# Optimization experiments

Measured on AMD Instinct MI355X. Metric: run time of the kernel, lower is better.

## Reference

```python
import jax, jax.numpy as jnp
import numpy as np

D_MODEL = 1024
N_HEADS = 16
HEAD_DIM = D_MODEL // N_HEADS


def setup_inputs() -> dict:
    key = jax.random.key(0)
    ks = jax.random.split(key, 5)
    B, S = 4, 2048
    scale = 1.0 / np.sqrt(D_MODEL)
    return {
        "x": jax.random.normal(ks[0], (B, S, D_MODEL), dtype=jnp.float32),
        "W_q": jax.random.normal(ks[1], (D_MODEL, D_MODEL), dtype=jnp.float32) * scale,
        "W_k": jax.random.normal(ks[2], (D_MODEL, D_MODEL), dtype=jnp.float32) * scale,
        "W_v": jax.random.normal(ks[3], (D_MODEL, D_MODEL), dtype=jnp.float32) * scale,
        "W_o": jax.random.normal(ks[4], (D_MODEL, D_MODEL), dtype=jnp.float32) * scale,
    }


def reference(x, W_q, W_k, W_v, W_o):
    B, S, _ = x.shape
    # nn.Linear(d,d,bias=False): y = x @ W.T ; W stored as (out,in)
    def proj(W):
        y = jnp.einsum('bsd,ed->bse', x, W)
        return y.reshape(B, S, N_HEADS, HEAD_DIM).transpose(0, 2, 1, 3)  # (B,H,S,Dh)
    q, k, v = proj(W_q), proj(W_k), proj(W_v)
    scores = jnp.einsum('bhqd,bhkd->bhqk', q, k) / np.sqrt(HEAD_DIM)
    causal = jnp.tril(jnp.ones((S, S), dtype=bool))  # (S,S)
    scores = jnp.where(causal[None, None], scores, -jnp.inf)
    attn = jax.nn.softmax(scores, axis=-1)
    heads = jnp.einsum('bhqk,bhkd->bhqd', attn, v)
    concat = heads.transpose(0, 2, 1, 3).reshape(B, S, D_MODEL)
    return jnp.einsum('bsd,ed->bse', concat, W_o)
```

## Files before the change

### kernel.cpp

```cpp
#include <hip/hip_runtime.h>
#include <hip/hip_bf16.h>

#define D_MODEL 1024
#define N_HEADS 16
#define HEAD_DIM 64
#define BATCH 4
#define SEQ 2048
#define M_ROWS (BATCH * SEQ)

typedef __attribute__((ext_vector_type(8))) __bf16 bf16x8;
typedef __attribute__((ext_vector_type(8))) short short8;
typedef __attribute__((ext_vector_type(4))) float f32x4;

static __device__ __forceinline__ unsigned short f2bf_rne(float f) {
  unsigned int u = __float_as_uint(f);
  u += 0x7FFFu + ((u >> 16) & 1u);
  return (unsigned short)(u >> 16);
}

#if __has_builtin(__builtin_amdgcn_exp2f)
#define EXP2F(x) __builtin_amdgcn_exp2f(x)
#else
#define EXP2F(x) exp2f(x)
#endif

static __device__ __forceinline__ void gl_lds16(const unsigned short* g, unsigned short* l) {
  __builtin_amdgcn_global_load_lds((const __attribute__((address_space(1))) unsigned int*)g,
                                   (__attribute__((address_space(3))) unsigned int*)l, 16, 0, 0);
}

#define BAR() asm volatile("s_barrier" ::: "memory")
#define WAIT_LGKM0() asm volatile("s_waitcnt lgkmcnt(0)" ::: "memory")
#define WAIT_VM(N) asm volatile("s_waitcnt vmcnt(" #N ")" ::: "memory")

__global__ __launch_bounds__(256) void cvt_all(const float* __restrict__ x,
                                               const float* __restrict__ wq,
                                               const float* __restrict__ wk,
                                               const float* __restrict__ wv,
                                               const float* __restrict__ wo,
                                               unsigned short* __restrict__ xb,
                                               unsigned short* __restrict__ wqb,
                                               unsigned short* __restrict__ wkb,
                                               unsigned short* __restrict__ wvb,
                                               unsigned short* __restrict__ wob) {
  const int bid = blockIdx.x;
  const float* src;
  unsigned short* dst;
  int i;
  if (bid < 8192) {
    src = x; dst = xb; i = bid * 256 + threadIdx.x;
  } else {
    int r = bid - 8192;
    int w = r >> 10;
    i = (r & 1023) * 256 + threadIdx.x;
    switch (w) {
      case 0: src = wq; dst = wqb; break;
      case 1: src = wk; dst = wkb; break;
      case 2: src = wv; dst = wvb; break;
      default: src = wo; dst = wob; break;
    }
  }
  float4 f = reinterpret_cast<const float4*>(src)[i];
  ushort4 o;
  o.x = f2bf_rne(f.x); o.y = f2bf_rne(f.y); o.z = f2bf_rne(f.z); o.w = f2bf_rne(f.w);
  reinterpret_cast<ushort4*>(dst)[i] = o;
}

__global__ __launch_bounds__(512, 2) void qkv_gemm8(const unsigned short* __restrict__ A,
                                                    const unsigned short* __restrict__ Wq,
                                                    const unsigned short* __restrict__ Wk,
                                                    const unsigned short* __restrict__ Wv,
                                                    unsigned short* __restrict__ Qo,
                                                    unsigned short* __restrict__ Ko,
                                                    unsigned short* __restrict__ Vt) {
  __shared__ __align__(16) unsigned short smem[65536];

  const int bid = blockIdx.x;
  const int wgid = (bid & 7) * 48 + (bid >> 3);
  const int widx = wgid >> 7;
  const int rem = wgid & 127;
  const int bm = rem >> 2, bn = rem & 3;

  const unsigned short* Bw = (widx == 0) ? Wq : (widx == 1) ? Wk : Wv;

  const int t = threadIdx.x;
  const int wave = t >> 6, lane = t & 63;
  const int wmi = wave >> 2, wni = wave & 3;
  const int lr = lane & 15, quad = lane >> 4;

  const int r0 = t >> 3, c0 = (t & 7) ^ (r0 & 7);
  const int s1 = t + 512;
  const int r1 = s1 >> 3, c1 = (s1 & 7) ^ (r1 & 7);
  const unsigned short* Asrc0 = A + (size_t)(bm * 256 + r0) * D_MODEL + c0 * 8;
  const unsigned short* Asrc1 = A + (size_t)(bm * 256 + r1) * D_MODEL + c1 * 8;
  const unsigned short* Bsrc0 = Bw + (size_t)(bn * 256 + r0) * D_MODEL + c0 * 8;
  const unsigned short* Bsrc1 = Bw + (size_t)(bn * 256 + r1) * D_MODEL + c1 * 8;

  auto stageA = [&](int kt, int buf, int half) {
    unsigned short* dst = &smem[(buf * 2 + half) * 8192];
    const size_t go = (size_t)half * (128 * D_MODEL) + kt * 64;
    gl_lds16(Asrc0 + go, dst + t * 8);
    gl_lds16(Asrc1 + go, dst + s1 * 8);
  };
  auto stageB = [&](int kt, int buf, int half) {
    unsigned short* dst = &smem[32768 + (buf * 2 + half) * 8192];
    const size_t go = (size_t)half * (128 * D_MODEL) + kt * 64;
    gl_lds16(Bsrc0 + go, dst + t * 8);
    gl_lds16(Bsrc1 + go, dst + s1 * 8);
  };

  f32x4 acc[8][4] = {};
  bf16x8 bfrag[4][2];

  stageA(0, 0, 0); stageA(0, 0, 1);
  stageB(0, 0, 0); stageB(0, 0, 1);
  stageB(1, 1, 0); stageB(1, 1, 1);
  WAIT_VM(4);
  BAR();

  const int brow0 = (wni & 1) * 64;
  for (int j = 0; j < 8; ++j) {
#pragma unroll
    for (int tb = 0; tb < 2; ++tb) {
      const unsigned short* As = &smem[(tb * 2 + wmi) * 8192];
      const unsigned short* Bs = &smem[32768 + (tb * 2 + (wni >> 1)) * 8192];
#pragma unroll
      for (int qd = 0; qd < 4; ++qd) {
        const int p = tb * 4 + qd;
        if (qd == 0) {
#pragma unroll
          for (int n = 0; n < 4; ++n)
#pragma unroll
            for (int ks = 0; ks < 2; ++ks) {
              const int row = brow0 + n * 16 + lr;
              bfrag[n][ks] = __builtin_bit_cast(
                  bf16x8, *reinterpret_cast<const short8*>(
                              &Bs[row * 64 + (((ks * 4 + quad) ^ (row & 7)) * 8)]));
            }
        }
        bf16x8 af[2][2];
#pragma unroll
        for (int mi = 0; mi < 2; ++mi)
#pragma unroll
          for (int ks = 0; ks < 2; ++ks) {
            const int row = (qd * 2 + mi) * 16 + lr;
            af[mi][ks] = __builtin_bit_cast(
                bf16x8, *reinterpret_cast<const short8*>(
                            &As[row * 64 + (((ks * 4 + quad) ^ (row & 7)) * 8)]));
          }
        if (p == 0) stageA(2 * j + 1, 1, 0);
        if (p == 1) { stageA(2 * j + 1, 1, 1); if (j < 7) stageB(2 * j + 2, 0, 0); }
        if (p == 2) { if (j < 7) stageB(2 * j + 2, 0, 1); }
        if (p == 4) { if (j < 7) stageA(2 * j + 2, 0, 0); }
        if (p == 5) { if (j < 7) { stageA(2 * j + 2, 0, 1); stageB(2 * j + 3, 1, 0); } }
        if (p == 6) { if (j < 7) stageB(2 * j + 3, 1, 1); }
        BAR();
        WAIT_LGKM0();
        __builtin_amdgcn_s_setprio(1);
#pragma unroll
        for (int mi = 0; mi < 2; ++mi)
#pragma unroll
          for (int n = 0; n < 4; ++n)
#pragma unroll
            for (int ks = 0; ks < 2; ++ks)
              acc[qd * 2 + mi][n] = __builtin_amdgcn_mfma_f32_16x16x32_bf16(
                  af[mi][ks], bfrag[n][ks], acc[qd * 2 + mi][n], 0, 0, 0);
        __builtin_amdgcn_s_setprio(0);
        if (p == 3) { if (j < 7) { WAIT_VM(4); } else { WAIT_VM(0); } }
        if (p == 7) { if (j < 7) { WAIT_VM(4); } }
        BAR();
      }
    }
  }

  if (widx < 2) {
    unsigned short* Cp = (widx == 0) ? Qo : Ko;
    const float sc = (widx == 0) ? 0.18033688f : 1.0f;
#pragma unroll
    for (int m = 0; m < 8; ++m) {
#pragma unroll
      for (int n = 0; n < 4; ++n) {
        const int col = bn * 256 + wni * 64 + n * 16 + lr;
#pragma unroll
        for (int r = 0; r < 4; ++r) {
          const int row = bm * 256 + wmi * 128 + m * 16 + quad * 4 + r;
          Cp[(size_t)row * D_MODEL + col] = f2bf_rne(acc[m][n][r] * sc);
        }
      }
    }
  } else {
    const int b = bm >> 3;
    const int s0 = (bm & 7) * 256;
#pragma unroll
    for (int h = 0; h < 2; ++h) {
      __syncthreads();
      if (wmi == h) {
#pragma unroll
        for (int n = 0; n < 4; ++n) {
          const int d = wni * 64 + n * 16 + lr;
#pragma unroll
          for (int m = 0; m < 8; ++m) {
#pragma unroll
            for (int r = 0; r < 4; ++r) {
              const int srow = m * 16 + quad * 4 + r;
              smem[d * 136 + srow] = f2bf_rne(acc[m][n][r]);
            }
          }
        }
      }
      __syncthreads();
#pragma unroll
      for (int i = 0; i < 8; ++i) {
        const int c = i * 512 + t;
        const int d = c >> 4, s8 = (c & 15) * 8;
        uint4 v = *reinterpret_cast<const uint4*>(&smem[d * 136 + s8]);
        const int h2 = bn * 4 + (d >> 6);
        const size_t rowbase = (size_t)(b * N_HEADS + h2) * HEAD_DIM + (d & 63);
        *reinterpret_cast<uint4*>(Vt + rowbase * SEQ + s0 + h * 128 + s8) = v;
      }
    }
  }
}

__global__ __launch_bounds__(256) void gemm_bt_f32(const unsigned short* __restrict__ A,
                                                   const unsigned short* __restrict__ Bw,
                                                   float* __restrict__ Cp,
                                                   int M, int N, int K) {
  __shared__ __align__(16) unsigned short smem[16384];
  const int t = threadIdx.x;
  const int bn = blockIdx.x, bm = blockIdx.y;
  const int wave = t >> 6, lane = t & 63;
  const int wm = (wave >> 1) * 64, wn = (wave & 1) * 64;
  const int lr = lane & 15, quad = lane >> 4;
  const int rxor = (lr >> 1) & 3;

  const int g0 = wave * 128 + lane, g1 = g0 + 64;
  const int r0 = g0 >> 2, c0 = (((g0 & 3) ^ ((r0 >> 1) & 3)) << 3);
  const int r1 = g1 >> 2, c1 = (((g1 & 3) ^ ((r1 >> 1) & 3)) << 3);
  const unsigned short* Arow0 = A + (size_t)(bm * 128 + r0) * K + c0;
  const unsigned short* Arow1 = A + (size_t)(bm * 128 + r1) * K + c1;
  const unsigned short* Brow0 = Bw + (size_t)(bn * 128 + r0) * K + c0;
  const unsigned short* Brow1 = Bw + (size_t)(bn * 128 + r1) * K + c1;

  f32x4 acc[4][4] = {};

  gl_lds16(Arow0, &smem[g0 * 8]);
  gl_lds16(Arow1, &smem[g1 * 8]);
  gl_lds16(Brow0, &smem[4096 + g0 * 8]);
  gl_lds16(Brow1, &smem[4096 + g1 * 8]);
  __syncthreads();

  for (int it = 0; it < 32; it++) {
    const int cur = (it & 1) * 8192;
    if (it + 1 < 32) {
      const int nxt = 8192 - cur;
      const int k1 = (it + 1) * 32;
      gl_lds16(Arow0 + k1, &smem[nxt + g0 * 8]);
      gl_lds16(Arow1 + k1, &smem[nxt + g1 * 8]);
      gl_lds16(Brow0 + k1, &smem[nxt + 4096 + g0 * 8]);
      gl_lds16(Brow1 + k1, &smem[nxt + 4096 + g1 * 8]);
    }
    const unsigned short* As = &smem[cur];
    const unsigned short* Bs = &smem[cur + 4096];

    bf16x8 af[4], bfr[4];
#pragma unroll
    for (int mt = 0; mt < 4; mt++)
      af[mt] = __builtin_bit_cast(
          bf16x8,
          *reinterpret_cast<const short8*>(&As[(wm + mt * 16 + lr) * 32 + (quad ^ rxor) * 8]));
#pragma unroll
    for (int nt = 0; nt < 4; nt++)
      bfr[nt] = __builtin_bit_cast(
          bf16x8,
          *reinterpret_cast<const short8*>(&Bs[(wn + nt * 16 + lr) * 32 + (quad ^ rxor) * 8]));
#pragma unroll
    for (int mt = 0; mt < 4; mt++)
#pragma unroll
      for (int nt = 0; nt < 4; nt++)
        acc[mt][nt] = __builtin_amdgcn_mfma_f32_16x16x32_bf16(af[mt], bfr[nt], acc[mt][nt], 0, 0, 0);
    __syncthreads();
  }

#pragma unroll
  for (int mt = 0; mt < 4; mt++) {
#pragma unroll
    for (int nt = 0; nt < 4; nt++) {
      int col = bn * 128 + wn + nt * 16 + lr;
#pragma unroll
      for (int r = 0; r < 4; r++) {
        int row = bm * 128 + wm + mt * 16 + quad * 4 + r;
        Cp[(size_t)row * N + col] = acc[mt][nt][r];
      }
    }
  }
}

__global__ __launch_bounds__(512, 4) void attn_causal(const unsigned short* __restrict__ Q,
                                                      const unsigned short* __restrict__ Km,
                                                      const unsigned short* __restrict__ Vt,
                                                      unsigned short* __restrict__ O) {
  __shared__ __align__(16) unsigned short Kv[2][2][64 * 64];
  __shared__ __align__(16) unsigned short Ps[8][16 * 72];

  const int bid = blockIdx.x;
  const int p = bid & 7;
  const int h = (bid >> 3) & 15;
  const int b = bid >> 7;

  const int t = threadIdx.x;
  const int wave = t >> 6, lane = t & 63;
  const int lr = lane & 15, quad = lane >> 4;
  const int cxor = lr & 7;

  const size_t base = (size_t)b * SEQ * D_MODEL + h * HEAD_DIM;
  const unsigned short* Qb = Q + base;
  const unsigned short* Kb = Km + base;
  const unsigned short* Vb = Vt + (size_t)(b * N_HEADS + h) * HEAD_DIM * SEQ;
  unsigned short* pw = &Ps[wave][0];

  const int srow = t >> 3;
  const int scol = ((t & 7) ^ (srow & 7)) << 3;
  const unsigned short* Kg = Kb + (size_t)srow * D_MODEL + scol;
  const unsigned short* Vg = Vb + (size_t)srow * SEQ + scol;

  for (int ph = 0; ph < 2; ph++) {
    const int qt = ph ? (15 - p) : p;
    const int m0 = qt * 128 + wave * 16;
    const int ntiles = (qt + 1) * 2;

    bf16x8 qf[2];
#pragma unroll
    for (int kk = 0; kk < 2; kk++)
      qf[kk] = __builtin_bit_cast(
          bf16x8,
          *reinterpret_cast<const short8*>(Qb + (size_t)(m0 + lr) * D_MODEL + kk * 32 + quad * 8));

    f32x4 o_acc[4] = {};
    float lsum[4] = {};

    gl_lds16(Kg, &Kv[0][0][t * 8]);
    gl_lds16(Vg, &Kv[0][1][t * 8]);

    for (int kt = 0; kt < ntiles; kt++) {
      const int cur = kt & 1;
      const int kv0 = kt * 64;
      __syncthreads();
      if (kt + 1 < ntiles) {
        gl_lds16(Kg + (size_t)(kv0 + 64) * D_MODEL, &Kv[1 - cur][0][t * 8]);
        gl_lds16(Vg + kv0 + 64, &Kv[1 - cur][1][t * 8]);
      }
      const unsigned short* Ks = &Kv[cur][0][0];
      const unsigned short* Vs = &Kv[cur][1][0];

      f32x4 sAcc[4] = {};
      __builtin_amdgcn_s_setprio(1);
#pragma unroll
      for (int kk = 0; kk < 2; kk++) {
        bf16x8 kf[4];
#pragma unroll
        for (int j = 0; j < 4; j++)
          kf[j] = __builtin_bit_cast(
              bf16x8, *reinterpret_cast<const short8*>(
                          &Ks[(j * 16 + lr) * 64 + ((kk * 4 + quad) ^ cxor) * 8]));
#pragma unroll
        for (int j = 0; j < 4; j++)
          sAcc[j] = __builtin_amdgcn_mfma_f32_16x16x32_bf16(qf[kk], kf[j], sAcc[j], 0, 0, 0);
      }
      __builtin_amdgcn_s_setprio(0);

      asm volatile("s_waitcnt lgkmcnt(0)" ::: "memory");
      const bool needmask = (kv0 + 63 > m0);
#pragma unroll
      for (int r = 0; r < 4; r++) {
        const int qpos = m0 + quad * 4 + r;
        float e[4];
#pragma unroll
        for (int j = 0; j < 4; j++) e[j] = EXP2F(sAcc[j][r]);
        if (needmask) {
#pragma unroll
          for (int j = 0; j < 4; j++)
            if (kv0 + j * 16 + lr > qpos) e[j] = 0.f;
        }
        lsum[r] += (e[0] + e[1]) + (e[2] + e[3]);
        unsigned short* pr = &pw[(quad * 4 + r) * 72];
#pragma unroll
        for (int j = 0; j < 4; j++) pr[j * 16 + lr] = f2bf_rne(e[j]);
      }
      asm volatile("s_waitcnt lgkmcnt(0)" ::: "memory");

      __builtin_amdgcn_s_setprio(1);
#pragma unroll
      for (int kk = 0; kk < 2; kk++) {
        bf16x8 pf = __builtin_bit_cast(
            bf16x8, *reinterpret_cast<const short8*>(&pw[lr * 72 + kk * 32 + quad * 8]));
#pragma unroll
        for (int c = 0; c < 4; c++) {
          bf16x8 vv = __builtin_bit_cast(
              bf16x8, *reinterpret_cast<const short8*>(
                          &Vs[(c * 16 + lr) * 64 + ((kk * 4 + quad) ^ cxor) * 8]));
          o_acc[c] = __builtin_amdgcn_mfma_f32_16x16x32_bf16(pf, vv, o_acc[c], 0, 0, 0);
        }
      }
      __builtin_amdgcn_s_setprio(0);
    }

#pragma unroll
    for (int r = 0; r < 4; r++) {
      float l = lsum[r];
#pragma unroll
      for (int off = 1; off < 16; off <<= 1) l += __shfl_xor(l, off, 64);
      const float inv = 1.f / l;
      const int qpos = m0 + quad * 4 + r;
#pragma unroll
      for (int c = 0; c < 4; c++)
        O[base + (size_t)qpos * D_MODEL + c * 16 + lr] = f2bf_rne(o_acc[c][r] * inv);
    }
  }
}

extern "C" void kernel_launch(void* const* d_in, const int* in_sizes, int n_in,
                              void* d_out, int out_size, void* d_ws, size_t ws_size,
                              hipStream_t stream) {
  const float* x  = (const float*)d_in[0];
  const float* Wq = (const float*)d_in[1];
  const float* Wk = (const float*)d_in[2];
  const float* Wv = (const float*)d_in[3];
  const float* Wo = (const float*)d_in[4];
  float* out = (float*)d_out;

  char* ws = (char*)d_ws;
  const size_t SZ_X = (size_t)M_ROWS * D_MODEL * 2;
  const size_t SZ_W = (size_t)D_MODEL * D_MODEL * 2;
  unsigned short* xb  = (unsigned short*)(ws);
  unsigned short* wqb = (unsigned short*)(ws + SZ_X);
  unsigned short* wkb = (unsigned short*)(ws + SZ_X + 1 * SZ_W);
  unsigned short* wvb = (unsigned short*)(ws + SZ_X + 2 * SZ_W);
  unsigned short* wob = (unsigned short*)(ws + SZ_X + 3 * SZ_W);
  unsigned short* Qb  = (unsigned short*)(ws + 1 * SZ_X + 4 * SZ_W);
  unsigned short* Kb  = (unsigned short*)(ws + 2 * SZ_X + 4 * SZ_W);
  unsigned short* Vt  = (unsigned short*)(ws + 3 * SZ_X + 4 * SZ_W);
  unsigned short* Ob  = xb;

  cvt_all<<<12288, 256, 0, stream>>>(x, Wq, Wk, Wv, Wo, xb, wqb, wkb, wvb, wob);

  qkv_gemm8<<<384, 512, 0, stream>>>(xb, wqb, wkb, wvb, Qb, Kb, Vt);

  attn_causal<<<512, 512, 0, stream>>>(Qb, Kb, Vt, Ob);

  gemm_bt_f32<<<dim3(8, 64), 256, 0, stream>>>(Ob, wob, out, M_ROWS, D_MODEL, D_MODEL);
}
```

Measured before the change: 245.9 us.

## Transpose QK^T MFMA output so P is written with packed bf16 stores, remap blocks to XCDs

Swaps the MFMA operand order so each lane holds four consecutive key positions for one query row. The exp values can then be packed with v_cvt_pk_bf16_f32 and written to a swizzled LDS P buffer as 8-byte stores, instead of 16 scalar 2-byte stores with rounding done in ALU code. Row sums become a single per-lane accumulator, reduced with two shuffles and redistributed at the end. Block indices are also remapped so each XCD handles a contiguous set of batch-head pairs, aiming at better L2 reuse of K/V. This risks mask and indexing mistakes in the new lane-to-row mapping.

```diff
diff --git a/kernel.cpp b/kernel.cpp
--- a/kernel.cpp
+++ b/kernel.cpp
@@ -16,6 +16,12 @@
   unsigned int u = __float_as_uint(f);
   u += 0x7FFFu + ((u >> 16) & 1u);
   return (unsigned short)(u >> 16);
+}
+
+static __device__ __forceinline__ unsigned int cvtpk_bf16(float a, float b) {
+  unsigned int r;
+  asm("v_cvt_pk_bf16_f32 %0, %1, %2" : "=v"(r) : "v"(a), "v"(b));
+  return r;
 }
 
 #if __has_builtin(__builtin_amdgcn_exp2f)
@@ -301,12 +307,14 @@
                                                       const unsigned short* __restrict__ Vt,
                                                       unsigned short* __restrict__ O) {
   __shared__ __align__(16) unsigned short Kv[2][2][64 * 64];
-  __shared__ __align__(16) unsigned short Ps[8][16 * 72];
+  __shared__ __align__(16) unsigned short Ps[8][1024];
 
   const int bid = blockIdx.x;
-  const int p = bid & 7;
-  const int h = (bid >> 3) & 15;
-  const int b = bid >> 7;
+  const int xcd = bid & 7, g = bid >> 3;
+  const int p = g >> 3;
+  const int bh = xcd * 8 + (g & 7);
+  const int h = bh & 15;
+  const int b = bh >> 4;
 
   const int t = threadIdx.x;
   const int wave = t >> 6, lane = t & 63;
@@ -337,7 +345,7 @@
           *reinterpret_cast<const short8*>(Qb + (size_t)(m0 + lr) * D_MODEL + kk * 32 + quad * 8));
 
     f32x4 o_acc[4] = {};
-    float lsum[4] = {};
+    float lsum = 0.f;
 
     gl_lds16(Kg, &Kv[0][0][t * 8]);
     gl_lds16(Vg, &Kv[0][1][t * 8]);
@@ -365,35 +373,39 @@
                           &Ks[(j * 16 + lr) * 64 + ((kk * 4 + quad) ^ cxor) * 8]));
 #pragma unroll
         for (int j = 0; j < 4; j++)
-          sAcc[j] = __builtin_amdgcn_mfma_f32_16x16x32_bf16(qf[kk], kf[j], sAcc[j], 0, 0, 0);
+          sAcc[j] = __builtin_amdgcn_mfma_f32_16x16x32_bf16(kf[j], qf[kk], sAcc[j], 0, 0, 0);
       }
       __builtin_amdgcn_s_setprio(0);
 
-      asm volatile("s_waitcnt lgkmcnt(0)" ::: "memory");
+      WAIT_LGKM0();
       const bool needmask = (kv0 + 63 > m0);
-#pragma unroll
-      for (int r = 0; r < 4; r++) {
-        const int qpos = m0 + quad * 4 + r;
+      const int kbase = kv0 - m0 + quad * 4;
+#pragma unroll
+      for (int j = 0; j < 4; j++) {
         float e[4];
 #pragma unroll
-        for (int j = 0; j < 4; j++) e[j] = EXP2F(sAcc[j][r]);
+        for (int r = 0; r < 4; r++) e[r] = EXP2F(sAcc[j][r]);
         if (needmask) {
 #pragma unroll
-          for (int j = 0; j < 4; j++)
-            if (kv0 + j * 16 + lr > qpos) e[j] = 0.f;
+          for (int r = 0; r < 4; r++)
+            if (kbase + 16 * j + r > lr) e[r] = 0.f;
         }
-        lsum[r] += (e[0] + e[1]) + (e[2] + e[3]);
-        unsigned short* pr = &pw[(quad * 4 + r) * 72];
-#pragma unroll
-        for (int j = 0; j < 4; j++) pr[j * 16 + lr] = f2bf_rne(e[j]);
-      }
-      asm volatile("s_waitcnt lgkmcnt(0)" ::: "memory");
+        lsum += (e[0] + e[1]) + (e[2] + e[3]);
+        const unsigned int pk0 = cvtpk_bf16(e[0], e[1]);
+        const unsigned int pk1 = cvtpk_bf16(e[2], e[3]);
+        const int c = 4 * j + quad;
+        *reinterpret_cast<uint2*>(
+            &pw[lr * 64 + (((c >> 1) ^ (lr & 7)) << 3) + ((c & 1) << 2)]) =
+            make_uint2(pk0, pk1);
+      }
+      WAIT_LGKM0();
 
       __builtin_amdgcn_s_setprio(1);
 #pragma unroll
       for (int kk = 0; kk < 2; kk++) {
         bf16x8 pf = __builtin_bit_cast(
-            bf16x8, *reinterpret_cast<const short8*>(&pw[lr * 72 + kk * 32 + quad * 8]));
+            bf16x8, *reinterpret_cast<const short8*>(
+                        &pw[lr * 64 + (((kk * 4 + quad) ^ (lr & 7)) << 3)]));
 #pragma unroll
         for (int c = 0; c < 4; c++) {
           bf16x8 vv = __builtin_bit_cast(
@@ -405,12 +417,13 @@
       __builtin_amdgcn_s_setprio(0);
     }
 
+    float l = lsum;
+    l += __shfl_xor(l, 16, 64);
+    l += __shfl_xor(l, 32, 64);
 #pragma unroll
     for (int r = 0; r < 4; r++) {
-      float l = lsum[r];
-#pragma unroll
-      for (int off = 1; off < 16; off <<= 1) l += __shfl_xor(l, off, 64);
-      const float inv = 1.f / l;
+      const float lq = __shfl(l, quad * 4 + r, 16);
+      const float inv = 1.f / lq;
       const int qpos = m0 + quad * 4 + r;
 #pragma unroll
       for (int c = 0; c < 4; c++)
```

Measured after the change: 233.7 us. 1.05x faster.
